# Performance work log

Hardware: AMD Instinct MI355X
Metric: run time of the kernel (lower is better)

The kernel has to match this reference:

```python
import jax, jax.numpy as jnp
import numpy as np

T, B = 64, 256
VOCAB, D, H = 32000, 512, 1024


def setup_inputs() -> dict:
    key = jax.random.key(0)
    k1, k2, k3, k4 = jax.random.split(key, 4)
    x = jax.random.randint(k1, (T, B), 0, VOCAB)  # token 0 = padding
    embed = jax.random.normal(k2, (VOCAB, D), dtype=jnp.float32)
    w_i = jax.random.normal(k3, (D, 3 * H), dtype=jnp.float32) / np.sqrt(D)
    w_h = jax.random.normal(k4, (H, 3 * H), dtype=jnp.float32) / np.sqrt(H)
    b = jnp.zeros((3 * H,), dtype=jnp.float32)
    return {"x": x, "embed": embed, "w_i": w_i, "w_h": w_h, "b": b}


def reference(x, embed, w_i, w_h, b):
    # Embed and mask out padding token 0.  words: [T, B, D]
    words = embed[x] * (x > 0).astype(embed.dtype)[..., None]
    h_dim = w_h.shape[0]
    w_h_zr, w_h_a = w_h[:, : 2 * h_dim], w_h[:, 2 * h_dim :]
    b_zr, b_a = b[: 2 * h_dim], b[2 * h_dim :]

    def step(h, w_t):
        gx = w_t @ w_i  # [B, 3H]
        zr_x, a_x = gx[..., : 2 * h_dim], gx[..., 2 * h_dim :]
        zr = jax.nn.sigmoid(zr_x + h @ w_h_zr + b_zr)
        z, r = zr[..., :h_dim], zr[..., h_dim:]
        a = jnp.tanh(a_x + (r * h) @ w_h_a + b_a)
        h_new = (1.0 - z) * h + z * a
        return h_new, h_new

    h0 = jnp.zeros((x.shape[1], h_dim), dtype=embed.dtype)
    _, seq = jax.lax.scan(step, h0, words)  # seq: [T, B, H]
    return seq.sum(0)  # compress == 'sum' -> [B, H]
```

## Files before the change

### kernel.cpp

```cpp
#include <hip/hip_runtime.h>
#include <hip/hip_bf16.h>
#include <stdint.h>


#define TT 64
#define BB 256
#define DD 512
#define HH 1024
#define N3H 3072
#define SLAB (BB * HH)

using frag  = __attribute__((ext_vector_type(8))) short;
using f32x4 = __attribute__((ext_vector_type(4))) float;

__device__ __forceinline__ uint16_t f2b(float f) {
    uint32_t u = __builtin_bit_cast(uint32_t, f);
    uint32_t r = u + 0x7FFFu + ((u >> 16) & 1u);
    return (uint16_t)(r >> 16);
}
__device__ __forceinline__ float b2f(uint16_t b) {
    uint32_t u = ((uint32_t)b) << 16;
    return __builtin_bit_cast(float, u);
}

__device__ __forceinline__ void load8_issue(const uint16_t* p, frag* f) {
    asm volatile(
        "global_load_dwordx4 %0, %8, off sc0 sc1\n\t"
        "global_load_dwordx4 %1, %8, off offset:64 sc0 sc1\n\t"
        "global_load_dwordx4 %2, %8, off offset:128 sc0 sc1\n\t"
        "global_load_dwordx4 %3, %8, off offset:192 sc0 sc1\n\t"
        "global_load_dwordx4 %4, %8, off offset:256 sc0 sc1\n\t"
        "global_load_dwordx4 %5, %8, off offset:320 sc0 sc1\n\t"
        "global_load_dwordx4 %6, %8, off offset:384 sc0 sc1\n\t"
        "global_load_dwordx4 %7, %8, off offset:448 sc0 sc1"
        : "=&v"(f[0]), "=&v"(f[1]), "=&v"(f[2]), "=&v"(f[3]),
          "=&v"(f[4]), "=&v"(f[5]), "=&v"(f[6]), "=&v"(f[7])
        : "v"(p)
        : "memory");
}

#define WAIT8(N, F)                                                       \
    asm volatile("s_waitcnt vmcnt(" #N ")"                                \
                 : "+v"((F)[0]), "+v"((F)[1]), "+v"((F)[2]),              \
                   "+v"((F)[3]), "+v"((F)[4]), "+v"((F)[5]),              \
                   "+v"((F)[6]), "+v"((F)[7]))

#define ZCON(KB, HF)                                                              \
    _Pragma("unroll")                                                             \
    for (int j = 0; j < 8; ++j) {                                                 \
        int kk = (KB) * 8 + j;                                                    \
        frag b0 = *(const frag*)(Wh + (l16)      * LDW + kk * 32 + quad * 8);     \
        frag b1 = *(const frag*)(Wh + (16 + l16) * LDW + kk * 32 + quad * 8);     \
        acc0 = __builtin_amdgcn_mfma_f32_16x16x32_bf16((HF)[j], b0, acc0, 0, 0, 0); \
        acc1 = __builtin_amdgcn_mfma_f32_16x16x32_bf16((HF)[j], b1, acc1, 0, 0, 0); \
    }

#define ACON(KB, RF)                                                              \
    _Pragma("unroll")                                                             \
    for (int j = 0; j < 8; ++j) {                                                 \
        int kk = (KB) * 8 + j;                                                    \
        frag b2 = *(const frag*)(Wh + (32 + l16) * LDW + kk * 32 + quad * 8);     \
        acc2 = __builtin_amdgcn_mfma_f32_16x16x32_bf16((RF)[j], b2, acc2, 0, 0, 0); \
    }


__global__ __launch_bounds__(256) void k_gather(const int* __restrict__ x,
                                                const float* __restrict__ embed,
                                                uint16_t* __restrict__ words) {
    int tid = blockIdx.x * 256 + threadIdx.x;
    int row = tid >> 6;
    int c8  = (tid & 63) << 3;
    int tok = x[row];
    float s = (tok > 0) ? 1.f : 0.f;
    const float4* src = (const float4*)(embed + (int64_t)tok * DD + c8);
    float4 v0 = src[0], v1 = src[1];
    float vals[8] = {v0.x, v0.y, v0.z, v0.w, v1.x, v1.y, v1.z, v1.w};
    union { uint16_t u[8]; uint4 q; } pk;
#pragma unroll
    for (int i = 0; i < 8; ++i) pk.u[i] = f2b(vals[i] * s);
    *(uint4*)(words + ((int64_t)row << 9) + c8) = pk.q;
}

__global__ void k_transpose(const float* __restrict__ src, uint16_t* __restrict__ dst,
                            int K, int N) {
    __shared__ float tile[32][33];
    int n0 = blockIdx.x * 32, k0 = blockIdx.y * 32;
    int tx = threadIdx.x, ty = threadIdx.y;
#pragma unroll
    for (int i = 0; i < 32; i += 8)
        tile[ty + i][tx] = src[(int64_t)(k0 + ty + i) * N + n0 + tx];
    __syncthreads();
#pragma unroll
    for (int i = 0; i < 32; i += 8)
        dst[(int64_t)(n0 + ty + i) * K + k0 + tx] = f2b(tile[tx][ty + i]);
}

__global__ void k_zero(uint4* p, int n16) {
    int i = blockIdx.x * blockDim.x + threadIdx.x;
    if (i < n16) p[i] = uint4{0u, 0u, 0u, 0u};
}


__global__ __launch_bounds__(256) void k_gemm_gx(const uint16_t* __restrict__ A,
                                                 const uint16_t* __restrict__ BT,
                                                 const float* __restrict__ bias,
                                                 uint16_t* __restrict__ C) {
    __shared__ uint16_t As[128][72];
    __shared__ uint16_t Bs[128][72];
    int m0 = blockIdx.y * 128;
    int n0 = blockIdx.x * 128;
    int t = threadIdx.x;
    int wave = t >> 6, lane = t & 63, quad = lane >> 4, l16 = lane & 15;
    int wm = (wave & 1) * 64, wn = (wave >> 1) * 64;
    f32x4 acc[4][4] = {};

    int sr = t >> 1;
    int sc = (t & 1) * 32;

    for (int k0 = 0; k0 < DD; k0 += 64) {
        const uint4* ga = (const uint4*)(A + (int64_t)(m0 + sr) * DD + k0 + sc);
        uint4 a0 = ga[0], a1 = ga[1], a2 = ga[2], a3 = ga[3];
        const uint4* gb = (const uint4*)(BT + (int64_t)(n0 + sr) * DD + k0 + sc);
        uint4 b0 = gb[0], b1 = gb[1], b2 = gb[2], b3 = gb[3];
        __syncthreads();
        *(uint4*)&As[sr][sc]      = a0;
        *(uint4*)&As[sr][sc + 8]  = a1;
        *(uint4*)&As[sr][sc + 16] = a2;
        *(uint4*)&As[sr][sc + 24] = a3;
        *(uint4*)&Bs[sr][sc]      = b0;
        *(uint4*)&Bs[sr][sc + 8]  = b1;
        *(uint4*)&Bs[sr][sc + 16] = b2;
        *(uint4*)&Bs[sr][sc + 24] = b3;
        __syncthreads();
#pragma unroll
        for (int kk = 0; kk < 64; kk += 32) {
            frag af[4], bf[4];
#pragma unroll
            for (int mi = 0; mi < 4; ++mi)
                af[mi] = *(const frag*)&As[wm + mi * 16 + l16][kk + quad * 8];
#pragma unroll
            for (int ni = 0; ni < 4; ++ni)
                bf[ni] = *(const frag*)&Bs[wn + ni * 16 + l16][kk + quad * 8];
#pragma unroll
            for (int mi = 0; mi < 4; ++mi)
#pragma unroll
                for (int ni = 0; ni < 4; ++ni)
                    acc[mi][ni] = __builtin_amdgcn_mfma_f32_16x16x32_bf16(
                        af[mi], bf[ni], acc[mi][ni], 0, 0, 0);
        }
    }
#pragma unroll
    for (int ni = 0; ni < 4; ++ni) {
        int col = n0 + wn + ni * 16 + l16;
        float bv = bias[col];
#pragma unroll
        for (int mi = 0; mi < 4; ++mi)
#pragma unroll
            for (int r = 0; r < 4; ++r) {
                int row = m0 + wm + mi * 16 + quad * 4 + r;
                C[(int64_t)row * N3H + col] = f2b(acc[mi][ni][r] + bv);
            }
    }
}


template <bool ROT>
__global__ __launch_bounds__(256, 1) void k_recur(const uint16_t* __restrict__ gx,
                                                  const uint16_t* __restrict__ wht,
                                                  uint16_t* __restrict__ hb,
                                                  uint16_t* __restrict__ rb,
                                                  unsigned int* __restrict__ bar,
                                                  float* __restrict__ out) {
    extern __shared__ uint16_t Wh[];
    const int LDW = HH + 8;
    int mg = blockIdx.x;
    int jb = blockIdx.y;
    int j0 = jb * 16;
    int m0 = mg * 64;
    int t = threadIdx.x, wave = t >> 6, lane = t & 63, quad = lane >> 4, l16 = lane & 15;

    for (int c = t; c < 48 * 128; c += 256) {
        int row = c >> 7;
        int off = (c & 127) << 3;
        int s = row >> 4, i = row & 15;
        *(uint4*)(Wh + row * LDW + off) =
            *(const uint4*)(wht + (int64_t)(s * HH + j0 + i) * HH + off);
    }
    __syncthreads();

    float hp[4]   = {0.f, 0.f, 0.f, 0.f};
    float zg[4];
    float osum[4] = {0.f, 0.f, 0.f, 0.f};
    int brow = m0 + wave * 16 + quad * 4;
    int jcol = j0 + l16;
    const int jc4 = j0 + (l16 & ~3);
    unsigned int* flags = bar + mg * 1024;
    unsigned int phase = 0;

    const int64_t arow = (int64_t)(m0 + wave * 16 + l16) * HH + quad * 8;

    auto bar_arrive = [&]() {
        __syncthreads();
        if (t == 0)
            (void)__hip_atomic_fetch_add(&flags[jb * 16], 1u, __ATOMIC_RELAXED,
                                         __HIP_MEMORY_SCOPE_AGENT);
    };
    auto bar_wait = [&](unsigned int ph) {
        if (wave == 0) {
            long guard = 0;
            for (;;) {
                unsigned int v = __hip_atomic_load(&flags[lane * 16], __ATOMIC_RELAXED,
                                                   __HIP_MEMORY_SCOPE_AGENT);
                if (__all((int)(v >= ph))) break;
                __builtin_amdgcn_s_sleep(1);
                if (++guard > (1L << 13)) break;
            }
        }
        __syncthreads();
    };

    auto store4 = [&](uint16_t* base, int r, uint32_t mine) {
        uint32_t p2 = mine | (((uint32_t)__shfl_xor((int)mine, 1)) << 16);
        uint32_t hi = (uint32_t)__shfl_xor((int)p2, 2);
        if ((l16 & 3) == 0) {
            uint64_t p4 = (uint64_t)p2 | ((uint64_t)hi << 32);
            uint64_t* dst = (uint64_t*)base + (int64_t)(brow + r) * (HH / 4) + (jc4 >> 2);
            asm volatile("global_store_dwordx2 %0, %1, off sc0 sc1"
                         :: "v"(dst), "v"(p4) : "memory");
        }
    };

    for (int step = 0; step < TT; ++step) {
        const uint16_t* hsrc;  uint16_t* rhdst;
        const uint16_t* rhsrc; uint16_t* hdst;
        if constexpr (ROT) {
            hsrc  = hb + (size_t)step * SLAB;
            hdst  = hb + (size_t)(step + 1) * SLAB;
            rhsrc = rb + (size_t)step * SLAB;
            rhdst = rb + (size_t)step * SLAB;
        } else {
            hsrc = hb; hdst = hb; rhsrc = rb; rhdst = rb;
        }

        if (step > 0) bar_arrive();

        uint16_t gzv[4], grv[4], gav[4];
        {
            const uint16_t* gxrow = gx + (int64_t)step * BB * N3H;
#pragma unroll
            for (int r = 0; r < 4; ++r) {
                const uint16_t* g = gxrow + (int64_t)(brow + r) * N3H + jcol;
                gzv[r] = g[0]; grv[r] = g[HH]; gav[r] = g[2 * HH];
            }
        }

        if (step > 0) bar_wait(++phase);

        {
            f32x4 acc0 = {}, acc1 = {};
            if constexpr (ROT) {
                const uint16_t* hrow = hsrc + arow;
#pragma unroll
                for (int kb = 0; kb < 4; ++kb) {
                    frag hf[8];
#pragma unroll
                    for (int j = 0; j < 8; ++j)
                        hf[j] = *(const frag*)(hrow + kb * 256 + j * 32);
                    ZCON(kb, hf);
                }
            } else {
                asm volatile("s_waitcnt vmcnt(0)" ::: "memory");
                const uint16_t* hrow = hsrc + arow;
                frag h0[8], h1[8], h2[8], h3[8];
                load8_issue(hrow,       h0);
                load8_issue(hrow + 256, h1);
                load8_issue(hrow + 512, h2);
                load8_issue(hrow + 768, h3);
                WAIT8(24, h0); ZCON(0, h0);
                WAIT8(16, h1); ZCON(1, h1);
                WAIT8(8,  h2); ZCON(2, h2);
                WAIT8(0,  h3); ZCON(3, h3);
            }
#pragma unroll
            for (int r = 0; r < 4; ++r) {
                float zp = b2f(gzv[r]) + acc0[r];
                float rp = b2f(grv[r]) + acc1[r];
                float z  = 1.f / (1.f + __expf(-zp));
                float rg = 1.f / (1.f + __expf(-rp));
                zg[r] = z;
                store4(rhdst, r, (uint32_t)f2b(rg * hp[r]));
            }
        }

        bar_arrive();
        bar_wait(++phase);

        {
            f32x4 acc2 = {};
            if constexpr (ROT) {
                const uint16_t* rrow = rhsrc + arow;
#pragma unroll
                for (int kb = 0; kb < 4; ++kb) {
                    frag rf[8];
#pragma unroll
                    for (int j = 0; j < 8; ++j)
                        rf[j] = *(const frag*)(rrow + kb * 256 + j * 32);
                    ACON(kb, rf);
                }
            } else {
                asm volatile("s_waitcnt vmcnt(0)" ::: "memory");
                const uint16_t* rrow = rhsrc + arow;
                frag rf0[8], rf1[8], rf2[8], rf3[8];
                load8_issue(rrow,       rf0);
                load8_issue(rrow + 256, rf1);
                load8_issue(rrow + 512, rf2);
                load8_issue(rrow + 768, rf3);
                WAIT8(24, rf0); ACON(0, rf0);
                WAIT8(16, rf1); ACON(1, rf1);
                WAIT8(8,  rf2); ACON(2, rf2);
                WAIT8(0,  rf3); ACON(3, rf3);
            }
#pragma unroll
            for (int r = 0; r < 4; ++r) {
                float a  = tanhf(b2f(gav[r]) + acc2[r]);
                float hn = (1.f - zg[r]) * hp[r] + zg[r] * a;
                osum[r] += hn;
                hp[r] = hn;
                store4(hdst, r, (uint32_t)f2b(hn));
            }
        }
    }
#pragma unroll
    for (int r = 0; r < 4; ++r)
        out[(int64_t)(brow + r) * HH + jcol] = osum[r];
}


extern "C" void kernel_launch(void* const* d_in, const int* in_sizes, int n_in,
                              void* d_out, int out_size, void* d_ws, size_t ws_size,
                              hipStream_t stream) {
    const int*   x     = (const int*)d_in[0];
    const float* embed = (const float*)d_in[1];
    const float* w_i   = (const float*)d_in[2];
    const float* w_h   = (const float*)d_in[3];
    const float* bias  = (const float*)d_in[4];
    float* out = (float*)d_out;

    char* ws = (char*)d_ws;
    uint16_t* gx    = (uint16_t*)(ws);
    uint16_t* wit   = (uint16_t*)(ws + 100663296);
    uint16_t* wht   = (uint16_t*)(ws + 103809024);
    uint16_t* words = (uint16_t*)(ws + 110100480);
    uint16_t* hbuf  = (uint16_t*)(ws + 126877696);
    uint16_t* rhbuf = (uint16_t*)(ws + 127401984);
    unsigned int* flags = (unsigned int*)(ws + 127926272);
    const size_t ROT_BASE = 127942656;
    uint16_t* hrot  = (uint16_t*)(ws + ROT_BASE);
    uint16_t* rhrot = (uint16_t*)(ws + ROT_BASE + 65ull * 524288);
    const size_t ROT_NEED = ROT_BASE + (65ull + 64ull) * 524288;
    const bool rot = ws_size >= ROT_NEED;

    k_gather<<<4096, 256, 0, stream>>>(x, embed, words);
    k_transpose<<<dim3(96, 16), dim3(32, 8), 0, stream>>>(w_i, wit, DD, N3H);
    k_transpose<<<dim3(96, 32), dim3(32, 8), 0, stream>>>(w_h, wht, HH, N3H);
    k_zero<<<261, 256, 0, stream>>>((uint4*)(ws + 126877696), (1048576 + 16384) / 16);
    if (rot)
        k_zero<<<128, 256, 0, stream>>>((uint4*)hrot, 524288 / 16);
    k_gemm_gx<<<dim3(24, 128), 256, 0, stream>>>(words, wit, bias, gx);
    if (rot)
        k_recur<true><<<dim3(4, 64), 256, 48 * (HH + 8) * 2, stream>>>(
            gx, wht, hrot, rhrot, flags, out);
    else
        k_recur<false><<<dim3(4, 64), 256, 48 * (HH + 8) * 2, stream>>>(
            gx, wht, hbuf, rhbuf, flags, out);
}
```

Measured before the change: 892.7 us.

## Replace global barrier with per-chunk flag waits overlapped with h loads

In the ROT path, the full grid barrier wait before each recurrent matmul is replaced by fine-grained waits on the flags of the 16 producer blocks covering each 256-column K-chunk. Loads of a chunk are issued as soon as its producers have arrived and are overlapped with MFMA work on the previous chunk. The aim is to cut barrier latency on the serial 64-step recurrence by pipelining dependency waits with compute. Correctness depends on the flag layout matching chunk ownership and on the non-coherent loads seeing fresh data, since the explicit sc0 sc1 bits are dropped.

```diff
diff --git a/kernel.cpp b/kernel.cpp
--- a/kernel.cpp
+++ b/kernel.cpp
@@ -33,6 +33,21 @@
         "global_load_dwordx4 %5, %8, off offset:320 sc0 sc1\n\t"
         "global_load_dwordx4 %6, %8, off offset:384 sc0 sc1\n\t"
         "global_load_dwordx4 %7, %8, off offset:448 sc0 sc1"
+        : "=&v"(f[0]), "=&v"(f[1]), "=&v"(f[2]), "=&v"(f[3]),
+          "=&v"(f[4]), "=&v"(f[5]), "=&v"(f[6]), "=&v"(f[7])
+        : "v"(p)
+        : "memory");
+}
+__device__ __forceinline__ void load8c(const uint16_t* p, frag* f) {
+    asm volatile(
+        "global_load_dwordx4 %0, %8, off\n\t"
+        "global_load_dwordx4 %1, %8, off offset:64\n\t"
+        "global_load_dwordx4 %2, %8, off offset:128\n\t"
+        "global_load_dwordx4 %3, %8, off offset:192\n\t"
+        "global_load_dwordx4 %4, %8, off offset:256\n\t"
+        "global_load_dwordx4 %5, %8, off offset:320\n\t"
+        "global_load_dwordx4 %6, %8, off offset:384\n\t"
+        "global_load_dwordx4 %7, %8, off offset:448"
         : "=&v"(f[0]), "=&v"(f[1]), "=&v"(f[2]), "=&v"(f[3]),
           "=&v"(f[4]), "=&v"(f[5]), "=&v"(f[6]), "=&v"(f[7])
         : "v"(p)
@@ -218,6 +233,19 @@
         }
         __syncthreads();
     };
+    auto wait_chunk = [&](unsigned int ph, int c) {
+        const unsigned int* slot = flags + (c * 16 + l16) * 16;
+        long guard = 0;
+        for (;;) {
+            unsigned int v;
+            asm volatile("global_load_dword %0, %1, off sc0 sc1\n\t"
+                         "s_waitcnt vmcnt(0)"
+                         : "=v"(v) : "v"(slot) : "memory");
+            if (__all((int)(v >= ph))) break;
+            __builtin_amdgcn_s_sleep(1);
+            if (++guard > (1L << 13)) break;
+        }
+    };
 
     auto store4 = [&](uint16_t* base, int r, uint32_t mine) {
         uint32_t p2 = mine | (((uint32_t)__shfl_xor((int)mine, 1)) << 16);
@@ -254,21 +282,22 @@
             }
         }
 
-        if (step > 0) bar_wait(++phase);
-
         {
             f32x4 acc0 = {}, acc1 = {};
             if constexpr (ROT) {
+                const unsigned int phZ = 2u * (unsigned)step;
                 const uint16_t* hrow = hsrc + arow;
-#pragma unroll
-                for (int kb = 0; kb < 4; ++kb) {
-                    frag hf[8];
-#pragma unroll
-                    for (int j = 0; j < 8; ++j)
-                        hf[j] = *(const frag*)(hrow + kb * 256 + j * 32);
-                    ZCON(kb, hf);
-                }
+                frag h0[8], h1[8], h2[8], h3[8];
+                wait_chunk(phZ, 0); load8c(hrow,       h0);
+                wait_chunk(phZ, 1); load8c(hrow + 256, h1);
+                WAIT8(8, h0); ZCON(0, h0);
+                wait_chunk(phZ, 2); load8c(hrow + 512, h2);
+                WAIT8(8, h1); ZCON(1, h1);
+                wait_chunk(phZ, 3); load8c(hrow + 768, h3);
+                WAIT8(8, h2); ZCON(2, h2);
+                WAIT8(0, h3); ZCON(3, h3);
             } else {
+                if (step > 0) bar_wait(++phase);
                 asm volatile("s_waitcnt vmcnt(0)" ::: "memory");
                 const uint16_t* hrow = hsrc + arow;
                 frag h0[8], h1[8], h2[8], h3[8];
@@ -293,32 +322,34 @@
         }
 
         bar_arrive();
-        bar_wait(++phase);
 
         {
             f32x4 acc2 = {};
             if constexpr (ROT) {
+                const unsigned int phA = 2u * (unsigned)step + 1u;
                 const uint16_t* rrow = rhsrc + arow;
-#pragma unroll
-                for (int kb = 0; kb < 4; ++kb) {
-                    frag rf[8];
-#pragma unroll
-                    for (int j = 0; j < 8; ++j)
-                        rf[j] = *(const frag*)(rrow + kb * 256 + j * 32);
-                    ACON(kb, rf);
-                }
+                frag r0[8], r1[8], r2[8], r3[8];
+                wait_chunk(phA, 0); load8c(rrow,       r0);
+                wait_chunk(phA, 1); load8c(rrow + 256, r1);
+                WAIT8(8, r0); ACON(0, r0);
+                wait_chunk(phA, 2); load8c(rrow + 512, r2);
+                WAIT8(8, r1); ACON(1, r1);
+                wait_chunk(phA, 3); load8c(rrow + 768, r3);
+                WAIT8(8, r2); ACON(2, r2);
+                WAIT8(0, r3); ACON(3, r3);
             } else {
+                bar_wait(++phase);
                 asm volatile("s_waitcnt vmcnt(0)" ::: "memory");
                 const uint16_t* rrow = rhsrc + arow;
-                frag rf0[8], rf1[8], rf2[8], rf3[8];
-                load8_issue(rrow,       rf0);
-                load8_issue(rrow + 256, rf1);
-                load8_issue(rrow + 512, rf2);
-                load8_issue(rrow + 768, rf3);
-                WAIT8(24, rf0); ACON(0, rf0);
-                WAIT8(16, rf1); ACON(1, rf1);
-                WAIT8(8,  rf2); ACON(2, rf2);
-                WAIT8(0,  rf3); ACON(3, rf3);
+                frag r0[8], r1[8], r2[8], r3[8];
+                load8_issue(rrow,       r0);
+                load8_issue(rrow + 256, r1);
+                load8_issue(rrow + 512, r2);
+                load8_issue(rrow + 768, r3);
+                WAIT8(24, r0); ACON(0, r0);
+                WAIT8(16, r1); ACON(1, r1);
+                WAIT8(8,  r2); ACON(2, r2);
+                WAIT8(0,  r3); ACON(3, r3);
             }
 #pragma unroll
             for (int r = 0; r < 4; ++r) {
```

New measurement: 1.026 ms. 14.9% more time.
